# Kernel tuning notes

Measured on AMD Instinct MI355X. Metric: run time of the kernel, lower is better.

Reference implementation:

```python
import jax, jax.numpy as jnp
import numpy as np

B, L, C, H = 8, 16384, 128, 4
EPS = 1e-5


def setup_inputs() -> dict:
    key = jax.random.key(0)
    k1, k2, k3, k4 = jax.random.split(key, 4)
    return {
        "x": jax.random.normal(k1, (B, L, C), dtype=jnp.float32),
        "W_qkv": jax.random.normal(k2, (3 * C, C), dtype=jnp.float32) * (C ** -0.5),
        "W_out": jax.random.normal(k3, (C, C), dtype=jnp.float32) * (C ** -0.5),
        "b_out": jax.random.normal(k4, (C,), dtype=jnp.float32) * 0.01,
        "gn_w": jnp.ones((C,), dtype=jnp.float32),
        "gn_b": jnp.zeros((C,), dtype=jnp.float32),
    }


def reference(x, W_qkv, W_out, b_out, gn_w, gn_b):
    b, l, c = x.shape
    h = H
    d = c // h                      # dim_head
    scale = d ** -0.5
    xc = jnp.swapaxes(x, 1, 2)      # [b, c, l]
    # 1x1 conv == channel matmul
    qkv = jnp.einsum('oc,bcl->bol', W_qkv, xc)     # [b, 3c, l]
    q, k, v = jnp.split(qkv, 3, axis=1)
    q = q.reshape(b, h, d, l)
    k = k.reshape(b, h, d, l)
    v = v.reshape(b, h, d, l)
    q = jax.nn.softmax(q, axis=2) * scale          # softmax over head-dim
    k = jax.nn.softmax(k, axis=3)                  # softmax over length
    context = jnp.einsum('bhcj,bhdj->bhcd', k, v)  # [b, h, d, d]
    out = jnp.einsum('bhcd,bhdi->bhci', context, q)  # [b, h, d, l]
    out = out.reshape(b, h * d, l)
    out = jnp.einsum('oc,bcl->bol', W_out, out) + b_out[None, :, None]
    # GroupNorm(1, c): normalize over (channel, length) per sample
    mean = jnp.mean(out, axis=(1, 2), keepdims=True)
    var = jnp.var(out, axis=(1, 2), keepdims=True)
    out = (out - mean) * jax.lax.rsqrt(var + EPS)
    out = out * gn_w[None, :, None] + gn_b[None, :, None]
    return jnp.swapaxes(out, 1, 2)                 # [b, l, c]
```

## Files before the change

kernel.cpp:

```cpp
#include <hip/hip_runtime.h>

#define BATCH 8
#define SEQL 16384
#define NCH 128
#define NH 4
#define HD 32
#define GEPS 1e-5f

typedef __bf16 bf16x8 __attribute__((ext_vector_type(8)));
typedef __bf16 bf16x4 __attribute__((ext_vector_type(4)));
typedef float f32x4 __attribute__((ext_vector_type(4)));

#define WKV_B   0
#define WQ_B    65536
#define WO_B    98304
#define CTXB_B  131072
#define CTXF_B  196608
#define ZF_B    327680
#define GNS_B   331776
#define GNF_B   331840
#define ZERO_BYTES (131072 + 4096 + 64 + 64)


__global__ void k_prep(const float* __restrict__ wqkv, const float* __restrict__ wout,
                       char* __restrict__ wsb) {
    int i = blockIdx.x * 256 + threadIdx.x;
    __bf16* wkvb = (__bf16*)(wsb + WKV_B);
    __bf16* wqb  = (__bf16*)(wsb + WQ_B);
    __bf16* wob  = (__bf16*)(wsb + WO_B);
    if (i < 384 * 128) {
        int o = i >> 7, c = i & 127;
        __bf16 v = (__bf16)wqkv[i];
        if (o < 128) wqb[o * 128 + c] = v;
        else         wkvb[(o - 128) * 128 + c] = v;
    }
    if (i < 128 * 128) wob[i] = (__bf16)wout[i];
}

__global__ __launch_bounds__(256, 3) void k_pass1(const float* __restrict__ x,
                                                  char* __restrict__ wsb) {
    __shared__ __attribute__((aligned(16))) __bf16 xb[8352];
    __shared__ __attribute__((aligned(16))) __bf16 ekv[16464];
    const int t = threadIdx.x;
    const int lane = t & 63, wave = t >> 6;
    const int n16 = lane & 15, q = lane >> 4;
    const int batch = blockIdx.x >> 8, chunk = blockIdx.x & 255;
    const __bf16* __restrict__ wkvb = (const __bf16*)(wsb + WKV_B);

    const float* xg = x + (size_t)(batch * SEQL + chunk * 64) * NCH;
#pragma unroll
    for (int r = 0; r < 8; r++) {
        int e = t + r * 256;
        int tok = e >> 5, c4 = (e & 31) * 4;
        float4 v = ((const float4*)xg)[e];
        bf16x4 h; h.x = (__bf16)v.x; h.y = (__bf16)v.y; h.z = (__bf16)v.z; h.w = (__bf16)v.w;
        *(bf16x4*)&xb[(c4 >> 5) * 2088 + ((c4 >> 3) & 3) * 520 + tok * 8 + (c4 & 7)] = h;
    }
    __syncthreads();

    float zacc[4][4];
#pragma unroll
    for (int i = 0; i < 4; i++)
#pragma unroll
        for (int j = 0; j < 4; j++) zacc[i][j] = 0.f;

#pragma unroll
    for (int half = 0; half < 2; half++) {
        f32x4 kvacc[4][2];
#pragma unroll
        for (int i = 0; i < 4; i++)
#pragma unroll
            for (int j = 0; j < 2; j++) kvacc[i][j] = (f32x4){0.f, 0.f, 0.f, 0.f};
#pragma unroll
        for (int ks = 0; ks < 4; ks++) {
            bf16x8 aw_k[4];
#pragma unroll
            for (int mt = 0; mt < 4; mt++)
                aw_k[mt] = *(const bf16x8*)&wkvb[(wave * 64 + mt * 16 + n16) * 128 + ks * 32 + q * 8];
            bf16x8 b[2];
#pragma unroll
            for (int nl = 0; nl < 2; nl++)
                b[nl] = *(const bf16x8*)&xb[ks * 2088 + q * 520 + ((half * 2 + nl) * 16 + n16) * 8];
#pragma unroll
            for (int mt = 0; mt < 4; mt++)
#pragma unroll
                for (int nl = 0; nl < 2; nl++)
                    kvacc[mt][nl] = __builtin_amdgcn_mfma_f32_16x16x32_bf16(
                        aw_k[mt], b[nl], kvacc[mt][nl], 0, 0, 0);
        }
#pragma unroll
        for (int mt = 0; mt < 4; mt++)
#pragma unroll
            for (int nl = 0; nl < 2; nl++) {
                int tt = (half * 2 + nl) * 16 + n16;
                int base = (tt >> 5) * 8232 + ((tt >> 3) & 3) * 2056 + (tt & 7);
#pragma unroll
                for (int r = 0; r < 4; r++) {
                    float vv = kvacc[mt][nl][r];
                    if (wave < 2) { vv = __expf(vv); zacc[mt][r] += vv; }
                    int o = wave * 64 + mt * 16 + q * 4 + r;
                    ekv[base + o * 8] = (__bf16)vv;
                }
            }
    }
    __syncthreads();

    f32x4 ctxacc[2][2];
#pragma unroll
    for (int i = 0; i < 2; i++)
#pragma unroll
        for (int j = 0; j < 2; j++) ctxacc[i][j] = (f32x4){0.f, 0.f, 0.f, 0.f};
#pragma unroll
    for (int ks2 = 0; ks2 < 2; ks2++) {
        bf16x8 ea[2], vb[2];
#pragma unroll
        for (int ml = 0; ml < 2; ml++) {
            ea[ml] = *(const bf16x8*)&ekv[ks2 * 8232 + q * 2056 + (wave * 32 + ml * 16 + n16) * 8];
            vb[ml] = *(const bf16x8*)&ekv[ks2 * 8232 + q * 2056 + (128 + wave * 32 + ml * 16 + n16) * 8];
        }
#pragma unroll
        for (int ml = 0; ml < 2; ml++)
#pragma unroll
            for (int nl = 0; nl < 2; nl++)
                ctxacc[ml][nl] = __builtin_amdgcn_mfma_f32_16x16x32_bf16(
                    ea[ml], vb[nl], ctxacc[ml][nl], 0, 0, 0);
    }

    float* ctxf = (float*)(wsb + CTXF_B) + ((size_t)(batch * 4 + wave) * 32) * 32;
#pragma unroll
    for (int ml = 0; ml < 2; ml++)
#pragma unroll
        for (int nl = 0; nl < 2; nl++)
#pragma unroll
            for (int r = 0; r < 4; r++)
                atomicAdd(&ctxf[(ml * 16 + q * 4 + r) * 32 + nl * 16 + n16], ctxacc[ml][nl][r]);
    if (wave < 2) {
        float* Zf = (float*)(wsb + ZF_B) + batch * 128;
#pragma unroll
        for (int mt = 0; mt < 4; mt++)
#pragma unroll
            for (int r = 0; r < 4; r++) {
                float z = zacc[mt][r];
                z += __shfl_xor(z, 1); z += __shfl_xor(z, 2);
                z += __shfl_xor(z, 4); z += __shfl_xor(z, 8);
                if (n16 == 0) atomicAdd(&Zf[wave * 64 + mt * 16 + q * 4 + r], z);
            }
    }
}

__global__ void k_ctxnorm(char* __restrict__ wsb) {
    int i = blockIdx.x * 256 + threadIdx.x;
    if (i < BATCH * NH * HD * HD) {
        const float* ctxf = (const float*)(wsb + CTXF_B);
        const float* Zf = (const float*)(wsb + ZF_B);
        __bf16* ctxb = (__bf16*)(wsb + CTXB_B);
        int c = (i >> 5) & 31, h = (i >> 10) & 3, b = i >> 12;
        ctxb[i] = (__bf16)(ctxf[i] / Zf[b * 128 + h * 32 + c]);
    }
}

__global__ __launch_bounds__(256, 4) void k_pass2(const float* __restrict__ x,
                                                  const float* __restrict__ bout,
                                                  char* __restrict__ wsb,
                                                  float* __restrict__ out) {
    __shared__ __attribute__((aligned(16))) __bf16 xb[8352];
    __shared__ __attribute__((aligned(16))) __bf16 pB[8352];
    __shared__ float gred[8];
    const int t = threadIdx.x;
    const int lane = t & 63, wave = t >> 6;
    const int n16 = lane & 15, q = lane >> 4;
    const int batch = blockIdx.x >> 8, chunk = blockIdx.x & 255;
    const __bf16* __restrict__ wqb = (const __bf16*)(wsb + WQ_B);
    const __bf16* __restrict__ wob = (const __bf16*)(wsb + WO_B);
    const __bf16* __restrict__ ctxb = (const __bf16*)(wsb + CTXB_B);

    const size_t tok0 = (size_t)batch * SEQL + chunk * 64;
    const float* xg = x + tok0 * NCH;
#pragma unroll
    for (int r = 0; r < 8; r++) {
        int e = t + r * 256;
        int tok = e >> 5, c4 = (e & 31) * 4;
        float4 v = ((const float4*)xg)[e];
        bf16x4 h; h.x = (__bf16)v.x; h.y = (__bf16)v.y; h.z = (__bf16)v.z; h.w = (__bf16)v.w;
        *(bf16x4*)&xb[(c4 >> 5) * 2088 + ((c4 >> 3) & 3) * 520 + tok * 8 + (c4 & 7)] = h;
    }
    __syncthreads();

    f32x4 qacc[2][4];
#pragma unroll
    for (int i = 0; i < 2; i++)
#pragma unroll
        for (int j = 0; j < 4; j++) qacc[i][j] = (f32x4){0.f, 0.f, 0.f, 0.f};
#pragma unroll
    for (int ks = 0; ks < 4; ks++) {
        bf16x8 aq_k[2];
#pragma unroll
        for (int ml = 0; ml < 2; ml++)
            aq_k[ml] = *(const bf16x8*)&wqb[(wave * 32 + ml * 16 + n16) * 128 + ks * 32 + q * 8];
        bf16x8 b[4];
#pragma unroll
        for (int nt = 0; nt < 4; nt++)
            b[nt] = *(const bf16x8*)&xb[ks * 2088 + q * 520 + (nt * 16 + n16) * 8];
#pragma unroll
        for (int ml = 0; ml < 2; ml++)
#pragma unroll
            for (int nt = 0; nt < 4; nt++)
                qacc[ml][nt] = __builtin_amdgcn_mfma_f32_16x16x32_bf16(
                    aq_k[ml], b[nt], qacc[ml][nt], 0, 0, 0);
    }
#pragma unroll
    for (int nt = 0; nt < 4; nt++) {
        float ss = 0.f;
#pragma unroll
        for (int ml = 0; ml < 2; ml++)
#pragma unroll
            for (int r = 0; r < 4; r++) {
                float e = __expf(qacc[ml][nt][r]);
                qacc[ml][nt][r] = e;
                ss += e;
            }
        ss += __shfl_xor(ss, 16);
        ss += __shfl_xor(ss, 32);
        float inv = 0.17677669529663687f / ss;
#pragma unroll
        for (int ml = 0; ml < 2; ml++)
#pragma unroll
            for (int r = 0; r < 4; r++) qacc[ml][nt][r] *= inv;
    }
#pragma unroll
    for (int ml = 0; ml < 2; ml++)
#pragma unroll
        for (int nt = 0; nt < 4; nt++) {
            bf16x4 h;
            h.x = (__bf16)qacc[ml][nt][0]; h.y = (__bf16)qacc[ml][nt][1];
            h.z = (__bf16)qacc[ml][nt][2]; h.w = (__bf16)qacc[ml][nt][3];
            *(bf16x4*)&pB[wave * 2088 + (ml * 2 + (q >> 1)) * 520 +
                          (nt * 16 + n16) * 8 + (q & 1) * 4] = h;
        }
    __syncthreads();
    bf16x8 actx[2];
#pragma unroll
    for (int ml = 0; ml < 2; ml++)
        actx[ml] = *(const bf16x8*)&ctxb[((size_t)(batch * 4 + wave) * 32 + ml * 16 + n16) * 32 + q * 8];
    f32x4 aacc[2][4];
#pragma unroll
    for (int ml = 0; ml < 2; ml++)
#pragma unroll
        for (int nt = 0; nt < 4; nt++) {
            bf16x8 pb = *(const bf16x8*)&pB[wave * 2088 + q * 520 + (nt * 16 + n16) * 8];
            aacc[ml][nt] = __builtin_amdgcn_mfma_f32_16x16x32_bf16(
                actx[ml], pb, (f32x4){0.f, 0.f, 0.f, 0.f}, 0, 0, 0);
        }
    __bf16* attB = xb;
#pragma unroll
    for (int ml = 0; ml < 2; ml++)
#pragma unroll
        for (int nt = 0; nt < 4; nt++) {
            bf16x4 h;
            h.x = (__bf16)aacc[ml][nt][0]; h.y = (__bf16)aacc[ml][nt][1];
            h.z = (__bf16)aacc[ml][nt][2]; h.w = (__bf16)aacc[ml][nt][3];
            *(bf16x4*)&attB[wave * 2088 + (ml * 2 + (q >> 1)) * 520 +
                            (nt * 16 + n16) * 8 + (q & 1) * 4] = h;
        }
    __syncthreads();
    f32x4 oacc[2][4];
#pragma unroll
    for (int i = 0; i < 2; i++)
#pragma unroll
        for (int j = 0; j < 4; j++) oacc[i][j] = (f32x4){0.f, 0.f, 0.f, 0.f};
#pragma unroll
    for (int ks = 0; ks < 4; ks++) {
        bf16x8 ao_k[2];
#pragma unroll
        for (int ml = 0; ml < 2; ml++)
            ao_k[ml] = *(const bf16x8*)&wob[(wave * 32 + ml * 16 + n16) * 128 + ks * 32 + q * 8];
        bf16x8 b[4];
#pragma unroll
        for (int nt = 0; nt < 4; nt++)
            b[nt] = *(const bf16x8*)&attB[ks * 2088 + q * 520 + (nt * 16 + n16) * 8];
#pragma unroll
        for (int ml = 0; ml < 2; ml++)
#pragma unroll
            for (int nt = 0; nt < 4; nt++)
                oacc[ml][nt] = __builtin_amdgcn_mfma_f32_16x16x32_bf16(
                    ao_k[ml], b[nt], oacc[ml][nt], 0, 0, 0);
    }
    float4 bias[2];
#pragma unroll
    for (int ml = 0; ml < 2; ml++)
        bias[ml] = *(const float4*)&bout[wave * 32 + ml * 16 + q * 4];
    float s1 = 0.f, s2 = 0.f;
#pragma unroll
    for (int ml = 0; ml < 2; ml++)
#pragma unroll
        for (int nt = 0; nt < 4; nt++) {
            float4 vv;
            vv.x = oacc[ml][nt][0] + bias[ml].x;
            vv.y = oacc[ml][nt][1] + bias[ml].y;
            vv.z = oacc[ml][nt][2] + bias[ml].z;
            vv.w = oacc[ml][nt][3] + bias[ml].w;
            s1 += vv.x + vv.y + vv.z + vv.w;
            s2 += vv.x * vv.x + vv.y * vv.y + vv.z * vv.z + vv.w * vv.w;
            *(float4*)&out[(tok0 + nt * 16 + n16) * NCH + wave * 32 + ml * 16 + q * 4] = vv;
        }
#pragma unroll
    for (int off = 32; off > 0; off >>= 1) {
        s1 += __shfl_xor(s1, off);
        s2 += __shfl_xor(s2, off);
    }
    if (lane == 0) { gred[wave * 2 + 0] = s1; gred[wave * 2 + 1] = s2; }
    __syncthreads();
    if (t < 2) {
        float s = gred[t] + gred[2 + t] + gred[4 + t] + gred[6 + t];
        atomicAdd(&((float*)(wsb + GNS_B))[batch * 2 + t], s);
    }
}

__global__ void k_gnfinal(char* __restrict__ wsb) {
    int b = threadIdx.x;
    if (b < BATCH) {
        const float n = (float)NCH * (float)SEQL;
        const float* gns = (const float*)(wsb + GNS_B);
        float* gnf = (float*)(wsb + GNF_B);
        float mean = gns[b * 2] / n;
        float var = gns[b * 2 + 1] / n - mean * mean;
        gnf[b * 2] = mean;
        gnf[b * 2 + 1] = rsqrtf(var + GEPS);
    }
}

__global__ __launch_bounds__(256) void k_gnorm(float* __restrict__ out,
                                               const char* __restrict__ wsb,
                                               const float* __restrict__ gw,
                                               const float* __restrict__ gb) {
    size_t i4 = (size_t)blockIdx.x * 256 + threadIdx.x;
    int b = (int)(i4 >> 19);
    int c4 = (int)(i4 & 31);
    const float* gnf = (const float*)(wsb + GNF_B);
    float mean = gnf[b * 2], rstd = gnf[b * 2 + 1];
    float4 w = *(const float4*)&gw[c4 * 4];
    float4 bb = *(const float4*)&gb[c4 * 4];
    float4 v = ((float4*)out)[i4];
    v.x = (v.x - mean) * rstd * w.x + bb.x;
    v.y = (v.y - mean) * rstd * w.y + bb.y;
    v.z = (v.z - mean) * rstd * w.z + bb.z;
    v.w = (v.w - mean) * rstd * w.w + bb.w;
    ((float4*)out)[i4] = v;
}

extern "C" void kernel_launch(void* const* d_in, const int* in_sizes, int n_in,
                              void* d_out, int out_size, void* d_ws, size_t ws_size,
                              hipStream_t stream) {
    const float* x    = (const float*)d_in[0];
    const float* wqkv = (const float*)d_in[1];
    const float* wout = (const float*)d_in[2];
    const float* bout = (const float*)d_in[3];
    const float* gw   = (const float*)d_in[4];
    const float* gb   = (const float*)d_in[5];
    float* out = (float*)d_out;
    char* wsb  = (char*)d_ws;

    hipMemsetAsync(wsb + CTXF_B, 0, ZERO_BYTES, stream);
    k_prep<<<192, 256, 0, stream>>>(wqkv, wout, wsb);
    k_pass1<<<2048, 256, 0, stream>>>(x, wsb);
    k_ctxnorm<<<128, 256, 0, stream>>>(wsb);
    k_pass2<<<2048, 256, 0, stream>>>(x, bout, wsb, out);
    k_gnfinal<<<1, 64, 0, stream>>>(wsb);
    k_gnorm<<<16384, 256, 0, stream>>>(out, wsb, gw, gb);
}
```

Measured before the change: 281.9 us.

## Replace context atomics with per-block partial slabs and a separate reduce kernel

Each k_pass1 block now writes its context and normalizer partial sums to its own workspace slab with plain stores, instead of issuing float atomicAdds into one shared per-batch buffer. A new k_reduce kernel sums the slabs and divides by Z. This removes the atomic contention and the memset of the accumulators. The kernel also hoists the K/V weight fragments into registers once per block and can loop over several chunks when workspace is small (P is chosen from ws_size). In exchange it writes and re-reads a large partial buffer (up to about 32MB), and the reduce kernel runs only 128 blocks, each looping serially over P slabs.

New measurement: 302.2 us. 7.2% more time.

```diff
diff --git a/kernel.cpp b/kernel.cpp
--- a/kernel.cpp
+++ b/kernel.cpp
@@ -15,11 +15,9 @@
 #define WQ_B    65536
 #define WO_B    98304
 #define CTXB_B  131072
-#define CTXF_B  196608
-#define ZF_B    327680
-#define GNS_B   331776
-#define GNF_B   331840
-#define ZERO_BYTES (131072 + 4096 + 64 + 64)
+#define GNS_B   196608
+#define GNF_B   196736
+#define CTXP_B  262144
 
 
 __global__ void k_prep(const float* __restrict__ wqkv, const float* __restrict__ wout,
@@ -38,104 +36,112 @@
 }
 
 __global__ __launch_bounds__(256, 3) void k_pass1(const float* __restrict__ x,
-                                                  char* __restrict__ wsb) {
+                                                  char* __restrict__ wsb, int P) {
     __shared__ __attribute__((aligned(16))) __bf16 xb[8352];
     __shared__ __attribute__((aligned(16))) __bf16 ekv[16464];
     const int t = threadIdx.x;
     const int lane = t & 63, wave = t >> 6;
     const int n16 = lane & 15, q = lane >> 4;
-    const int batch = blockIdx.x >> 8, chunk = blockIdx.x & 255;
+    const int batch = blockIdx.x / P, sub = blockIdx.x % P;
+    const int nrep = 256 / P;
     const __bf16* __restrict__ wkvb = (const __bf16*)(wsb + WKV_B);
 
-    const float* xg = x + (size_t)(batch * SEQL + chunk * 64) * NCH;
-#pragma unroll
-    for (int r = 0; r < 8; r++) {
-        int e = t + r * 256;
-        int tok = e >> 5, c4 = (e & 31) * 4;
-        float4 v = ((const float4*)xg)[e];
-        bf16x4 h; h.x = (__bf16)v.x; h.y = (__bf16)v.y; h.z = (__bf16)v.z; h.w = (__bf16)v.w;
-        *(bf16x4*)&xb[(c4 >> 5) * 2088 + ((c4 >> 3) & 3) * 520 + tok * 8 + (c4 & 7)] = h;
-    }
-    __syncthreads();
-
+    bf16x8 aw[4][4];
+#pragma unroll
+    for (int mt = 0; mt < 4; mt++)
+#pragma unroll
+        for (int ks = 0; ks < 4; ks++)
+            aw[mt][ks] = *(const bf16x8*)&wkvb[(wave * 64 + mt * 16 + n16) * 128 + ks * 32 + q * 8];
+
+    f32x4 ctxacc[2][2];
+#pragma unroll
+    for (int i = 0; i < 2; i++)
+#pragma unroll
+        for (int j = 0; j < 2; j++) ctxacc[i][j] = (f32x4){0.f, 0.f, 0.f, 0.f};
     float zacc[4][4];
 #pragma unroll
     for (int i = 0; i < 4; i++)
 #pragma unroll
         for (int j = 0; j < 4; j++) zacc[i][j] = 0.f;
 
-#pragma unroll
-    for (int half = 0; half < 2; half++) {
-        f32x4 kvacc[4][2];
-#pragma unroll
-        for (int i = 0; i < 4; i++)
-#pragma unroll
-            for (int j = 0; j < 2; j++) kvacc[i][j] = (f32x4){0.f, 0.f, 0.f, 0.f};
-#pragma unroll
-        for (int ks = 0; ks < 4; ks++) {
-            bf16x8 aw_k[4];
+    for (int rep = 0; rep < nrep; rep++) {
+        const int chunk = sub + rep * P;
+        const float* xg = x + (size_t)(batch * SEQL + chunk * 64) * NCH;
+#pragma unroll
+        for (int r = 0; r < 8; r++) {
+            int e = t + r * 256;
+            int tok = e >> 5, c4 = (e & 31) * 4;
+            float4 v = ((const float4*)xg)[e];
+            bf16x4 h; h.x = (__bf16)v.x; h.y = (__bf16)v.y; h.z = (__bf16)v.z; h.w = (__bf16)v.w;
+            *(bf16x4*)&xb[(c4 >> 5) * 2088 + ((c4 >> 3) & 3) * 520 + tok * 8 + (c4 & 7)] = h;
+        }
+        __syncthreads();
+
+#pragma unroll
+        for (int half = 0; half < 2; half++) {
+            f32x4 kvacc[4][2];
+#pragma unroll
+            for (int i = 0; i < 4; i++)
+#pragma unroll
+                for (int j = 0; j < 2; j++) kvacc[i][j] = (f32x4){0.f, 0.f, 0.f, 0.f};
+#pragma unroll
+            for (int ks = 0; ks < 4; ks++) {
+                bf16x8 b[2];
+#pragma unroll
+                for (int nl = 0; nl < 2; nl++)
+                    b[nl] = *(const bf16x8*)&xb[ks * 2088 + q * 520 + ((half * 2 + nl) * 16 + n16) * 8];
+#pragma unroll
+                for (int mt = 0; mt < 4; mt++)
+#pragma unroll
+                    for (int nl = 0; nl < 2; nl++)
+                        kvacc[mt][nl] = __builtin_amdgcn_mfma_f32_16x16x32_bf16(
+                            aw[mt][ks], b[nl], kvacc[mt][nl], 0, 0, 0);
+            }
 #pragma unroll
             for (int mt = 0; mt < 4; mt++)
-                aw_k[mt] = *(const bf16x8*)&wkvb[(wave * 64 + mt * 16 + n16) * 128 + ks * 32 + q * 8];
-            bf16x8 b[2];
-#pragma unroll
-            for (int nl = 0; nl < 2; nl++)
-                b[nl] = *(const bf16x8*)&xb[ks * 2088 + q * 520 + ((half * 2 + nl) * 16 + n16) * 8];
-#pragma unroll
-            for (int mt = 0; mt < 4; mt++)
+#pragma unroll
+                for (int nl = 0; nl < 2; nl++) {
+                    int tt = (half * 2 + nl) * 16 + n16;
+                    int base = (tt >> 5) * 8232 + ((tt >> 3) & 3) * 2056 + (tt & 7);
+#pragma unroll
+                    for (int r = 0; r < 4; r++) {
+                        float vv = kvacc[mt][nl][r];
+                        if (wave < 2) { vv = __expf(vv); zacc[mt][r] += vv; }
+                        int o = wave * 64 + mt * 16 + q * 4 + r;
+                        ekv[base + o * 8] = (__bf16)vv;
+                    }
+                }
+        }
+        __syncthreads();
+
+#pragma unroll
+        for (int ks2 = 0; ks2 < 2; ks2++) {
+            bf16x8 ea[2], vb[2];
+#pragma unroll
+            for (int ml = 0; ml < 2; ml++) {
+                ea[ml] = *(const bf16x8*)&ekv[ks2 * 8232 + q * 2056 + (wave * 32 + ml * 16 + n16) * 8];
+                vb[ml] = *(const bf16x8*)&ekv[ks2 * 8232 + q * 2056 + (128 + wave * 32 + ml * 16 + n16) * 8];
+            }
+#pragma unroll
+            for (int ml = 0; ml < 2; ml++)
 #pragma unroll
                 for (int nl = 0; nl < 2; nl++)
-                    kvacc[mt][nl] = __builtin_amdgcn_mfma_f32_16x16x32_bf16(
-                        aw_k[mt], b[nl], kvacc[mt][nl], 0, 0, 0);
-        }
-#pragma unroll
-        for (int mt = 0; mt < 4; mt++)
-#pragma unroll
-            for (int nl = 0; nl < 2; nl++) {
-                int tt = (half * 2 + nl) * 16 + n16;
-                int base = (tt >> 5) * 8232 + ((tt >> 3) & 3) * 2056 + (tt & 7);
-#pragma unroll
-                for (int r = 0; r < 4; r++) {
-                    float vv = kvacc[mt][nl][r];
-                    if (wave < 2) { vv = __expf(vv); zacc[mt][r] += vv; }
-                    int o = wave * 64 + mt * 16 + q * 4 + r;
-                    ekv[base + o * 8] = (__bf16)vv;
-                }
-            }
-    }
-    __syncthreads();
-
-    f32x4 ctxacc[2][2];
-#pragma unroll
-    for (int i = 0; i < 2; i++)
-#pragma unroll
-        for (int j = 0; j < 2; j++) ctxacc[i][j] = (f32x4){0.f, 0.f, 0.f, 0.f};
-#pragma unroll
-    for (int ks2 = 0; ks2 < 2; ks2++) {
-        bf16x8 ea[2], vb[2];
-#pragma unroll
-        for (int ml = 0; ml < 2; ml++) {
-            ea[ml] = *(const bf16x8*)&ekv[ks2 * 8232 + q * 2056 + (wave * 32 + ml * 16 + n16) * 8];
-            vb[ml] = *(const bf16x8*)&ekv[ks2 * 8232 + q * 2056 + (128 + wave * 32 + ml * 16 + n16) * 8];
-        }
-#pragma unroll
-        for (int ml = 0; ml < 2; ml++)
-#pragma unroll
-            for (int nl = 0; nl < 2; nl++)
-                ctxacc[ml][nl] = __builtin_amdgcn_mfma_f32_16x16x32_bf16(
-                    ea[ml], vb[nl], ctxacc[ml][nl], 0, 0, 0);
-    }
-
-    float* ctxf = (float*)(wsb + CTXF_B) + ((size_t)(batch * 4 + wave) * 32) * 32;
+                    ctxacc[ml][nl] = __builtin_amdgcn_mfma_f32_16x16x32_bf16(
+                        ea[ml], vb[nl], ctxacc[ml][nl], 0, 0, 0);
+        }
+        __syncthreads();
+    }
+
+    float* ctxp = (float*)(wsb + CTXP_B) + (size_t)blockIdx.x * 4096 + wave * 1024;
 #pragma unroll
     for (int ml = 0; ml < 2; ml++)
 #pragma unroll
         for (int nl = 0; nl < 2; nl++)
 #pragma unroll
             for (int r = 0; r < 4; r++)
-                atomicAdd(&ctxf[(ml * 16 + q * 4 + r) * 32 + nl * 16 + n16], ctxacc[ml][nl][r]);
+                ctxp[(ml * 16 + q * 4 + r) * 32 + nl * 16 + n16] = ctxacc[ml][nl][r];
     if (wave < 2) {
-        float* Zf = (float*)(wsb + ZF_B) + batch * 128;
+        float* zp = (float*)(wsb + CTXP_B) + (size_t)gridDim.x * 4096 + (size_t)blockIdx.x * 128;
 #pragma unroll
         for (int mt = 0; mt < 4; mt++)
 #pragma unroll
@@ -143,20 +149,25 @@
                 float z = zacc[mt][r];
                 z += __shfl_xor(z, 1); z += __shfl_xor(z, 2);
                 z += __shfl_xor(z, 4); z += __shfl_xor(z, 8);
-                if (n16 == 0) atomicAdd(&Zf[wave * 64 + mt * 16 + q * 4 + r], z);
+                if (n16 == 0) zp[wave * 64 + mt * 16 + q * 4 + r] = z;
             }
     }
 }
 
-__global__ void k_ctxnorm(char* __restrict__ wsb) {
+__global__ __launch_bounds__(256) void k_reduce(char* __restrict__ wsb, int P) {
     int i = blockIdx.x * 256 + threadIdx.x;
-    if (i < BATCH * NH * HD * HD) {
-        const float* ctxf = (const float*)(wsb + CTXF_B);
-        const float* Zf = (const float*)(wsb + ZF_B);
-        __bf16* ctxb = (__bf16*)(wsb + CTXB_B);
-        int c = (i >> 5) & 31, h = (i >> 10) & 3, b = i >> 12;
-        ctxb[i] = (__bf16)(ctxf[i] / Zf[b * 128 + h * 32 + c]);
-    }
+    int b = i >> 12, elem = i & 4095;
+    int hc = elem >> 5;
+    const float* ctxp = (const float*)(wsb + CTXP_B);
+    const float* zp = ctxp + (size_t)(BATCH * P) * 4096;
+    float cs = 0.f, zs = 0.f;
+    for (int p = 0; p < P; p++) {
+        size_t slab = (size_t)(b * P + p);
+        cs += ctxp[slab * 4096 + elem];
+        zs += zp[slab * 128 + hc];
+    }
+    __bf16* ctxb = (__bf16*)(wsb + CTXB_B);
+    ctxb[i] = (__bf16)(cs / zs);
 }
 
 __global__ __launch_bounds__(256, 4) void k_pass2(const float* __restrict__ x,
@@ -360,10 +371,15 @@
     float* out = (float*)d_out;
     char* wsb  = (char*)d_ws;
 
-    hipMemsetAsync(wsb + CTXF_B, 0, ZERO_BYTES, stream);
+    int P = 256;
+    while (P > 1 &&
+           (size_t)CTXP_B + (size_t)BATCH * P * (16384 + 512) > ws_size)
+        P >>= 1;
+
+    hipMemsetAsync(wsb + GNS_B, 0, 64, stream);
     k_prep<<<192, 256, 0, stream>>>(wqkv, wout, wsb);
-    k_pass1<<<2048, 256, 0, stream>>>(x, wsb);
-    k_ctxnorm<<<128, 256, 0, stream>>>(wsb);
+    k_pass1<<<BATCH * P, 256, 0, stream>>>(x, wsb, P);
+    k_reduce<<<128, 256, 0, stream>>>(wsb, P);
     k_pass2<<<2048, 256, 0, stream>>>(x, bout, wsb, out);
     k_gnfinal<<<1, 64, 0, stream>>>(wsb);
     k_gnorm<<<16384, 256, 0, stream>>>(out, wsb, gw, gb);
```
